# Kernel tuning notes

Hardware: AMD Instinct MI355X
Metric: run time of the kernel (lower is better)

The kernel has to match this reference:

```python
import jax, jax.numpy as jnp
import numpy as np
import math

N, C, W, H = 8, 1024, 1024, 16
D = C // H  # head size = 64


def setup_inputs() -> dict:
    key = jax.random.key(0)
    ks = jax.random.split(key, 7)
    s = 1.0 / math.sqrt(C)
    return {
        "hidden_states": jax.random.normal(ks[0], (N, C, W), jnp.float32),
        "attention_mask": jnp.zeros((N, 1, 1, W), jnp.float32),
        "wq": jax.random.normal(ks[1], (C, C), jnp.float32) * s,
        "bq": jax.random.normal(ks[2], (C,), jnp.float32) * 0.02,
        "wk": jax.random.normal(ks[3], (C, C), jnp.float32) * s,
        "bk": jax.random.normal(ks[4], (C,), jnp.float32) * 0.02,
        "wv": jax.random.normal(ks[5], (C, C), jnp.float32) * s,
        "bv": jax.random.normal(ks[6], (C,), jnp.float32) * 0.02,
    }


def reference(hidden_states, attention_mask, wq, bq, wk, bk, wv, bv):
    # conv1d(kernel=1, groups=1) == per-position GEMM: [N,C,W] x [Cout,Cin] -> [N,Cout,W]
    q = jnp.einsum('ncw,oc->now', hidden_states, wq) + bq[None, :, None]
    k = jnp.einsum('ncw,oc->now', hidden_states, wk) + bk[None, :, None]
    v = jnp.einsum('ncw,oc->now', hidden_states, wv) + bv[None, :, None]
    # split heads: [N,C,W] -> [N,H,D,W]
    q = q.reshape(N, H, D, W).transpose(0, 1, 3, 2)  # [N,H,W,D]
    k = k.reshape(N, H, D, W)                         # [N,H,D,W]
    v = v.reshape(N, H, D, W).transpose(0, 1, 3, 2)  # [N,H,W,D]
    scores = jnp.einsum('nhqd,nhdk->nhqk', q, k) / math.sqrt(D)
    scores = scores + attention_mask  # broadcast [N,1,1,W]
    probs = jax.nn.softmax(scores, axis=-1)
    ctx = jnp.einsum('nhqk,nhkd->nhqd', probs, v)    # [N,H,W,D]
    # merge heads back to [N,C,W]
    return ctx.transpose(0, 1, 3, 2).reshape(N, C, W)
```

## Files before the change

kernel.cpp:

```cpp
#include <hip/hip_runtime.h>
#include <hip/hip_bf16.h>

typedef __bf16 bf16x8 __attribute__((ext_vector_type(8)));
typedef __bf16 bf16x4 __attribute__((ext_vector_type(4)));
typedef float f32x4 __attribute__((ext_vector_type(4)));

#define N_ 8
#define C_ 1024
#define W_ 1024
#define H_ 16
#define D_ 64

typedef __attribute__((address_space(3))) void lds_void;
typedef const __attribute__((address_space(1))) void gbl_void;
static __device__ __forceinline__ void gload_lds16(const void* g, void* l) {
    __builtin_amdgcn_global_load_lds((gbl_void*)g, (lds_void*)l, 16, 0, 0);
}

__global__ __launch_bounds__(256)
void prep(const float* __restrict__ hs,
          const float* __restrict__ wq, const float* __restrict__ wk,
          const float* __restrict__ wv,
          __bf16* __restrict__ Xt, __bf16* __restrict__ Wb) {
    __shared__ float tile[64][68];
    const int b = blockIdx.x;
    const int t = threadIdx.x;
    if (b < 2048) {
        const int bx = b & 15, by = (b >> 4) & 15, bz = b >> 8;
        const long bin  = (long)bz * C_ * W_;
        const long bout = (long)bz * W_ * C_;
        const int w0 = bx * 64, c0 = by * 64;
        const int rr = t >> 4;
        const int cg = (t & 15) * 4;
        #pragma unroll
        for (int it = 0; it < 4; ++it) {
            const int cr = it * 16 + rr;
            f32x4 v = *(const f32x4*)(const void*)(hs + bin + (long)(c0 + cr) * W_ + w0 + cg);
            *(f32x4*)&tile[cr][cg] = v;
        }
        __syncthreads();
        #pragma unroll
        for (int it = 0; it < 4; ++it) {
            const int wr = it * 16 + rr;
            bf16x4 o;
            #pragma unroll
            for (int u = 0; u < 4; ++u) o[u] = (__bf16)tile[cg + u][wr];
            *(bf16x4*)(void*)(Xt + bout + (long)(w0 + wr) * C_ + c0 + cg) = o;
        }
    } else {
        const int cb = b - 2048;
        const int wsel = cb >> 9;
        const int x = cb & 511;
        const float* s = wsel == 0 ? wq : (wsel == 1 ? wk : wv);
        __bf16* d = Wb + (long)wsel * C_ * C_;
        const long i = ((long)x * 256 + t) * 8;
        f32x4 a = *(const f32x4*)(const void*)(s + i);
        f32x4 bb = *(const f32x4*)(const void*)(s + i + 4);
        bf16x8 v;
        #pragma unroll
        for (int u = 0; u < 4; ++u) { v[u] = (__bf16)a[u]; v[u + 4] = (__bf16)bb[u]; }
        *(bf16x8*)(void*)(d + i) = v;
    }
}

template<int OUT_T>
static __device__ __forceinline__
void gemm_body(const __bf16* __restrict__ Aw, const __bf16* __restrict__ Xn,
               const float* __restrict__ bias, __bf16* __restrict__ Pn,
               const int o0, const int w0, __bf16* __restrict__ Bs) {
    const int tid = threadIdx.x;
    const int wv = tid >> 6, lane = tid & 63;
    const int l15 = lane & 15, quad = lane >> 4;
    const int wr = (wv >> 1) * 64, wc = (wv & 1) * 64;
    const int lr4 = lane >> 2;
    const int lc4 = lane & 3;

    f32x4 acc[4][4] = {};

    auto stageB = [&](int k0, int b) {
        #pragma unroll
        for (int j = 0; j < 2; ++j) {
            const int seg = wv * 2 + j;
            const int r = seg * 16 + lr4;
            const int q = lc4 ^ ((lr4 >> 1) & 3);
            gload_lds16(Xn + (long)(w0 + r) * C_ + k0 + q * 8, Bs + b * 4096 + seg * 512);
        }
    };

    stageB(0, 0);
    stageB(32, 1);

    int cur = 0, nxt = 2;
    #pragma unroll 1
    for (int ti = 0; ti < 32; ++ti) {
        if (ti < 31) asm volatile("s_waitcnt vmcnt(2)" ::: "memory");
        else         asm volatile("s_waitcnt vmcnt(0)" ::: "memory");
        __builtin_amdgcn_s_barrier();
        asm volatile("" ::: "memory");

        const int k0 = ti * 32;
        bf16x8 af[4];
        #pragma unroll
        for (int mt = 0; mt < 4; ++mt) {
            const int R = o0 + wr + mt * 16 + l15;
            af[mt] = *(const bf16x8*)(const void*)(Aw + (long)R * C_ + k0 + quad * 8);
        }
        if (ti + 2 < 32) {
            stageB((ti + 2) * 32, nxt);
            nxt = nxt + 1 == 3 ? 0 : nxt + 1;
        }

        const __bf16* Bb = Bs + cur * 4096;
        bf16x8 bf[4];
        #pragma unroll
        for (int nt = 0; nt < 4; ++nt) {
            const int R = wc + nt * 16 + l15;
            const int pos = quad ^ ((R >> 1) & 3);
            bf[nt] = *(const bf16x8*)(const void*)&Bb[R * 32 + pos * 8];
        }
        #pragma unroll
        for (int mt = 0; mt < 4; ++mt)
            #pragma unroll
            for (int nt = 0; nt < 4; ++nt) {
                if (OUT_T == 0)
                    acc[mt][nt] = __builtin_amdgcn_mfma_f32_16x16x32_bf16(af[mt], bf[nt], acc[mt][nt], 0, 0, 0);
                else
                    acc[mt][nt] = __builtin_amdgcn_mfma_f32_16x16x32_bf16(bf[nt], af[mt], acc[mt][nt], 0, 0, 0);
            }
        cur = cur + 1 == 3 ? 0 : cur + 1;
    }

    #pragma unroll
    for (int mt = 0; mt < 4; ++mt) {
        #pragma unroll
        for (int nt = 0; nt < 4; ++nt) {
            #pragma unroll
            for (int rg = 0; rg < 4; ++rg) {
                if (OUT_T == 0) {
                    const int col = w0 + wc + nt * 16 + l15;
                    const int row = o0 + wr + mt * 16 + quad * 4 + rg;
                    Pn[(long)row * W_ + col] = (__bf16)(acc[mt][nt][rg] + bias[row]);
                } else {
                    const int o = o0 + wr + mt * 16 + l15;
                    const int w = w0 + wc + nt * 16 + quad * 4 + rg;
                    Pn[(long)w * C_ + o] = (__bf16)(acc[mt][nt][rg] + bias[o]);
                }
            }
        }
    }
}

__global__ __launch_bounds__(256)
void gemm_qkv(const __bf16* __restrict__ Wb, const __bf16* __restrict__ Xt,
              const float* __restrict__ bq, const float* __restrict__ bk,
              const float* __restrict__ bv,
              __bf16* __restrict__ Qt, __bf16* __restrict__ Kt,
              __bf16* __restrict__ Vb) {
    __shared__ __align__(16) __bf16 Bs[3 * 4096];
    const int f = blockIdx.x;
    const int n = f & 7;
    const int j = f >> 3;
    const int which = j >> 6;
    const int t = j & 63;
    const int o0 = (t >> 3) * 128;
    const int w0 = (t & 7) * 128;
    const size_t SZ = (size_t)C_ * W_;
    const size_t WSZ = (size_t)C_ * C_;
    const __bf16* Xn = Xt + (size_t)n * SZ;
    const __bf16* Aw = Wb + (size_t)which * WSZ;
    if (which < 2)
        gemm_body<1>(Aw, Xn, which ? bk : bq, (which ? Kt : Qt) + n * SZ, o0, w0, Bs);
    else
        gemm_body<0>(Aw, Xn, bv, Vb + n * SZ, o0, w0, Bs);
}

__global__ __launch_bounds__(256)
void flash_attn(const __bf16* __restrict__ Qt,
                const __bf16* __restrict__ Kt,
                const __bf16* __restrict__ V,
                const float* __restrict__ mask,
                float* __restrict__ out) {
    __shared__ __align__(16) __bf16 Pl[4 * 16 * 64];
    __shared__ __align__(16) __bf16 Ks[2][64 * 64];
    __shared__ __align__(16) __bf16 Vs[2][64 * 64];

    const int f = blockIdx.x;
    const int g = (f & 7) + ((f >> 6) << 3);
    const int m = (f >> 3) & 7;
    const int n = g >> 4, h = g & 15;
    const int q0 = m * 128;

    const int tid = threadIdx.x;
    const int wave = tid >> 6, lane = tid & 63;
    const int l15 = lane & 15, quad = lane >> 4;
    const int lr8 = lane >> 3, lp = lane & 7;
    const long nqk = (long)n * W_ * C_;
    const long nv = (long)n * C_ * W_;
    const int hD = h * D_;
    const float* mrow = mask + (long)n * W_;
    constexpr float SC = 0.125f * 1.44269504f;
    constexpr float L2E = 1.44269504f;

    char* plb = (char*)Pl + wave * 2048;
    const int swz = (l15 & 7) << 4;
    const int plrow = l15 * 128;

    bf16x8 aq[2][2];
    #pragma unroll
    for (int qs = 0; qs < 2; ++qs)
        #pragma unroll
        for (int dc = 0; dc < 2; ++dc)
            aq[qs][dc] = *(const bf16x8*)(const void*)
                (Qt + nqk + (long)(q0 + wave * 32 + qs * 16 + l15) * C_ + hD + dc * 32 + quad * 8);

    f32x4 o_acc[2][4] = {};
    float l_ln[2] = {};

    auto stageK = [&](int kt, int b) {
        #pragma unroll
        for (int jj = 0; jj < 2; ++jj) {
            const int seg = wave * 2 + jj;
            const int r = seg * 8 + lr8;
            const int q = lp ^ (r & 7);
            gload_lds16(Kt + nqk + (long)(kt + r) * C_ + hD + q * 8, &Ks[b][seg * 512]);
        }
    };
    auto stageV = [&](int kt, int b) {
        #pragma unroll
        for (int jj = 0; jj < 2; ++jj) {
            const int seg = wave * 2 + jj;
            const int r = seg * 8 + lr8;
            const int q = lp ^ (r & 7);
            gload_lds16(V + nv + (long)(hD + r) * W_ + kt + q * 8, &Vs[b][seg * 512]);
        }
    };

    stageK(0, 0);
    stageV(0, 0);

    #pragma unroll 1
    for (int ti = 0; ti < W_ / 64; ++ti) {
        const int kt = ti * 64;
        const int cur = ti & 1;

        asm volatile("s_waitcnt vmcnt(2)" ::: "memory");
        __builtin_amdgcn_s_barrier();
        asm volatile("" ::: "memory");
        if (ti + 1 < W_ / 64) stageK(kt + 64, cur ^ 1);

        bf16x8 bk[4][2];
        #pragma unroll
        for (int ks = 0; ks < 4; ++ks)
            #pragma unroll
            for (int dc = 0; dc < 2; ++dc) {
                const int R = ks * 16 + l15;
                const int pos = (dc * 4 + quad) ^ (R & 7);
                bk[ks][dc] = *(const bf16x8*)(const void*)&Ks[cur][R * 64 + pos * 8];
            }
        f32x4 mk2[4];
        #pragma unroll
        for (int ks = 0; ks < 4; ++ks) {
            f32x4 mv = *(const f32x4*)(const void*)(mrow + kt + ks * 16 + quad * 4);
            #pragma unroll
            for (int rg = 0; rg < 4; ++rg) mk2[ks][rg] = mv[rg] * L2E;
        }

        f32x4 s2[2][4] = {};
        #pragma unroll
        for (int qs = 0; qs < 2; ++qs)
            #pragma unroll
            for (int ks = 0; ks < 4; ++ks)
                #pragma unroll
                for (int dc = 0; dc < 2; ++dc)
                    s2[qs][ks] = __builtin_amdgcn_mfma_f32_16x16x32_bf16(bk[ks][dc], aq[qs][dc], s2[qs][ks], 0, 0, 0);

        #pragma unroll
        for (int qs = 0; qs < 2; ++qs)
            #pragma unroll
            for (int ks = 0; ks < 4; ++ks) {
                #pragma unroll
                for (int rg = 0; rg < 4; ++rg)
                    s2[qs][ks][rg] = __builtin_amdgcn_exp2f(s2[qs][ks][rg] * SC + mk2[ks][rg]);
                l_ln[qs] += (s2[qs][ks][0] + s2[qs][ks][1]) + (s2[qs][ks][2] + s2[qs][ks][3]);
            }

        bf16x8 ap[2][2];
        #pragma unroll
        for (int qs = 0; qs < 2; ++qs) {
            #pragma unroll
            for (int ks = 0; ks < 4; ++ks) {
                bf16x4 p4;
                #pragma unroll
                for (int rg = 0; rg < 4; ++rg) p4[rg] = (__bf16)s2[qs][ks][rg];
                *(bf16x4*)(void*)(plb + plrow + ((ks * 32 + quad * 8) ^ swz)) = p4;
            }
            #pragma unroll
            for (int kc = 0; kc < 2; ++kc)
                ap[qs][kc] = *(const bf16x8*)(const void*)
                    (plb + plrow + ((kc * 64 + quad * 16) ^ swz));
        }

        if (ti + 1 < W_ / 64) asm volatile("s_waitcnt vmcnt(2)" ::: "memory");
        else                  asm volatile("s_waitcnt vmcnt(0)" ::: "memory");
        __builtin_amdgcn_s_barrier();
        asm volatile("" ::: "memory");
        if (ti + 1 < W_ / 64) stageV(kt + 64, cur ^ 1);

        bf16x8 bv[4][2];
        #pragma unroll
        for (int ds = 0; ds < 4; ++ds)
            #pragma unroll
            for (int kc = 0; kc < 2; ++kc) {
                const int R = ds * 16 + l15;
                const int pos = (kc * 4 + quad) ^ (R & 7);
                bv[ds][kc] = *(const bf16x8*)(const void*)&Vs[cur][R * 64 + pos * 8];
            }
        #pragma unroll
        for (int qs = 0; qs < 2; ++qs)
            #pragma unroll
            for (int ds = 0; ds < 4; ++ds)
                #pragma unroll
                for (int kc = 0; kc < 2; ++kc)
                    o_acc[qs][ds] = __builtin_amdgcn_mfma_f32_16x16x32_bf16(ap[qs][kc], bv[ds][kc], o_acc[qs][ds], 0, 0, 0);
    }

    #pragma unroll
    for (int qs = 0; qs < 2; ++qs) {
        float l = l_ln[qs];
        l += __shfl_xor(l, 16, 64);
        l += __shfl_xor(l, 32, 64);
        const float linv = 1.0f / l;
        #pragma unroll
        for (int rg = 0; rg < 4; ++rg) {
            const float inv = __shfl(linv, quad * 4 + rg, 64);
            #pragma unroll
            for (int ds = 0; ds < 4; ++ds)
                out[nv + (long)(hD + ds * 16 + l15) * W_ + q0 + wave * 32 + qs * 16 + quad * 4 + rg]
                    = o_acc[qs][ds][rg] * inv;
        }
    }
}

extern "C" void kernel_launch(void* const* d_in, const int* in_sizes, int n_in,
                              void* d_out, int out_size, void* d_ws, size_t ws_size,
                              hipStream_t stream) {
    (void)in_sizes; (void)n_in; (void)out_size; (void)ws_size;
    const float* hs   = (const float*)d_in[0];
    const float* mask = (const float*)d_in[1];
    const float* wq   = (const float*)d_in[2];
    const float* bq   = (const float*)d_in[3];
    const float* wk   = (const float*)d_in[4];
    const float* bk   = (const float*)d_in[5];
    const float* wv   = (const float*)d_in[6];
    const float* bv   = (const float*)d_in[7];
    float* out = (float*)d_out;

    const size_t SZ = (size_t)N_ * C_ * W_;
    const size_t WSZ = (size_t)C_ * C_;
    __bf16* Wb = (__bf16*)d_ws;
    __bf16* Xt = Wb + 3 * WSZ;
    __bf16* Qt = Xt + SZ;
    __bf16* Kt = Qt + SZ;
    __bf16* Vb = Kt + SZ;

    prep<<<dim3(2048 + 1536), 256, 0, stream>>>(hs, wq, wk, wv, Xt, Wb);

    gemm_qkv<<<dim3(1536), 256, 0, stream>>>(Wb, Xt, bq, bk, bv, Qt, Kt, Vb);

    flash_attn<<<dim3(1024), 256, 0, stream>>>(Qt, Kt, Vb, mask, out);
}
```

Before: 272.7 us.

## Prefetch GEMM A fragments into registers with double-buffered LDS; raise MFMA priority

The QKV GEMM moves from a triple-buffered LDS ring (B tile staged two steps ahead, A fragments loaded from global inside each step) to a double buffer. The loop is unrolled by two and ping-pongs two register sets, so the A fragments for the next k-step are loaded while the current step runs. This hides A load latency and cuts LDS from 24KB to 16KB per block, which may allow more resident blocks, but B prefetch depth drops from two steps to one. The attention kernel also wraps its MFMA blocks in s_setprio(1)/s_setprio(0) so matrix work gets issue priority over other waves.

```diff
diff --git a/kernel.cpp b/kernel.cpp
--- a/kernel.cpp
+++ b/kernel.cpp
@@ -86,28 +86,25 @@
             gload_lds16(Xn + (long)(w0 + r) * C_ + k0 + q * 8, Bs + b * 4096 + seg * 512);
         }
     };
-
+    const __bf16* Ap = Aw + (long)(o0 + wr + l15) * C_ + quad * 8;
+    auto loadA = [&](int k0, bf16x8 (&af)[4]) {
+        #pragma unroll
+        for (int mt = 0; mt < 4; ++mt)
+            af[mt] = *(const bf16x8*)(const void*)(Ap + (long)(mt * 16) * C_ + k0);
+    };
+
+    bf16x8 afA[4], afB[4];
     stageB(0, 0);
-    stageB(32, 1);
-
-    int cur = 0, nxt = 2;
-    #pragma unroll 1
-    for (int ti = 0; ti < 32; ++ti) {
-        if (ti < 31) asm volatile("s_waitcnt vmcnt(2)" ::: "memory");
-        else         asm volatile("s_waitcnt vmcnt(0)" ::: "memory");
+    loadA(0, afA);
+
+    auto body = [&](int ti, bf16x8 (&afc)[4], bf16x8 (&afn)[4]) {
+        const int cur = ti & 1;
+        asm volatile("s_waitcnt vmcnt(4)" ::: "memory");
         __builtin_amdgcn_s_barrier();
         asm volatile("" ::: "memory");
-
-        const int k0 = ti * 32;
-        bf16x8 af[4];
-        #pragma unroll
-        for (int mt = 0; mt < 4; ++mt) {
-            const int R = o0 + wr + mt * 16 + l15;
-            af[mt] = *(const bf16x8*)(const void*)(Aw + (long)R * C_ + k0 + quad * 8);
-        }
-        if (ti + 2 < 32) {
-            stageB((ti + 2) * 32, nxt);
-            nxt = nxt + 1 == 3 ? 0 : nxt + 1;
+        if (ti + 1 < 32) {
+            stageB((ti + 1) * 32, cur ^ 1);
+            loadA((ti + 1) * 32, afn);
         }
 
         const __bf16* Bb = Bs + cur * 4096;
@@ -123,11 +120,16 @@
             #pragma unroll
             for (int nt = 0; nt < 4; ++nt) {
                 if (OUT_T == 0)
-                    acc[mt][nt] = __builtin_amdgcn_mfma_f32_16x16x32_bf16(af[mt], bf[nt], acc[mt][nt], 0, 0, 0);
+                    acc[mt][nt] = __builtin_amdgcn_mfma_f32_16x16x32_bf16(afc[mt], bf[nt], acc[mt][nt], 0, 0, 0);
                 else
-                    acc[mt][nt] = __builtin_amdgcn_mfma_f32_16x16x32_bf16(bf[nt], af[mt], acc[mt][nt], 0, 0, 0);
-            }
-        cur = cur + 1 == 3 ? 0 : cur + 1;
+                    acc[mt][nt] = __builtin_amdgcn_mfma_f32_16x16x32_bf16(bf[nt], afc[mt], acc[mt][nt], 0, 0, 0);
+            }
+    };
+
+    #pragma unroll 1
+    for (int tt = 0; tt < 16; ++tt) {
+        body(2 * tt,     afA, afB);
+        body(2 * tt + 1, afB, afA);
     }
 
     #pragma unroll
@@ -156,7 +158,7 @@
               const float* __restrict__ bv,
               __bf16* __restrict__ Qt, __bf16* __restrict__ Kt,
               __bf16* __restrict__ Vb) {
-    __shared__ __align__(16) __bf16 Bs[3 * 4096];
+    __shared__ __align__(16) __bf16 Bs[2 * 4096];
     const int f = blockIdx.x;
     const int n = f & 7;
     const int j = f >> 3;
@@ -266,6 +268,7 @@
         }
 
         f32x4 s2[2][4] = {};
+        __builtin_amdgcn_s_setprio(1);
         #pragma unroll
         for (int qs = 0; qs < 2; ++qs)
             #pragma unroll
@@ -273,6 +276,7 @@
                 #pragma unroll
                 for (int dc = 0; dc < 2; ++dc)
                     s2[qs][ks] = __builtin_amdgcn_mfma_f32_16x16x32_bf16(bk[ks][dc], aq[qs][dc], s2[qs][ks], 0, 0, 0);
+        __builtin_amdgcn_s_setprio(0);
 
         #pragma unroll
         for (int qs = 0; qs < 2; ++qs)
@@ -315,6 +319,7 @@
                 const int pos = (kc * 4 + quad) ^ (R & 7);
                 bv[ds][kc] = *(const bf16x8*)(const void*)&Vs[cur][R * 64 + pos * 8];
             }
+        __builtin_amdgcn_s_setprio(1);
         #pragma unroll
         for (int qs = 0; qs < 2; ++qs)
             #pragma unroll
@@ -322,6 +327,7 @@
                 #pragma unroll
                 for (int kc = 0; kc < 2; ++kc)
                     o_acc[qs][ds] = __builtin_amdgcn_mfma_f32_16x16x32_bf16(ap[qs][kc], bv[ds][kc], o_acc[qs][ds], 0, 0, 0);
+        __builtin_amdgcn_s_setprio(0);
     }
 
     #pragma unroll
```

Result: no change. 275.8 us (+1.1%).
